# Optimization experiments

Hardware: AMD Instinct MI355X
Metric: run time of the kernel (lower is better)

Reference implementation:

```python
import jax, jax.numpy as jnp
import numpy as np

H = 16  # num_heads

def setup_inputs() -> dict:
    key = jax.random.key(0)
    k1, k2, k3 = jax.random.split(key, 3)
    D = 1024
    x = jax.random.normal(k1, (4, 2048, D), dtype=jnp.float32)
    W_qkv = jax.random.normal(k2, (D, 3 * D), dtype=jnp.float32) * (1.0 / np.sqrt(D))
    b_qkv = jnp.zeros((3 * D,), dtype=jnp.float32)
    W_out = jax.random.normal(k3, (D, D), dtype=jnp.float32) * (1.0 / np.sqrt(D))
    b_out = jnp.zeros((D,), dtype=jnp.float32)
    return {"x": x, "W_qkv": W_qkv, "b_qkv": b_qkv, "W_out": W_out, "b_out": b_out}

def reference(x, W_qkv, b_qkv, W_out, b_out):
    B, S, D = x.shape
    hd = D // H  # head_dim
    qkv = x @ W_qkv + b_qkv  # [B,S,3D]
    q, k, v = jnp.split(qkv, 3, axis=-1)
    # [B,S,D] -> [B,H,S,hd]
    q = q.reshape(B, S, H, hd).transpose(0, 2, 1, 3)
    k = k.reshape(B, S, H, hd).transpose(0, 2, 1, 3)
    v = v.reshape(B, S, H, hd).transpose(0, 2, 1, 3)
    scores = jnp.einsum('bhqd,bhkd->bhqk', q, k) / jnp.sqrt(jnp.float32(hd))
    weights = jax.nn.softmax(scores, axis=-1)  # dropout p=0.0 (eval)
    out = jnp.einsum('bhqk,bhkd->bhqd', weights, v)
    out = out.transpose(0, 2, 1, 3).reshape(B, S, D)
    return out @ W_out + b_out
```

## Files before the change

### kernel.cpp

```cpp
#include <hip/hip_runtime.h>

typedef __bf16 bf16;
typedef __bf16 bf16x4 __attribute__((ext_vector_type(4)));
typedef __bf16 bf16x8 __attribute__((ext_vector_type(8)));
typedef short s16x4 __attribute__((ext_vector_type(4)));
typedef float f32x4 __attribute__((ext_vector_type(4)));

static constexpr int NB = 4;
static constexpr int NS = 2048;
static constexpr int ND = 1024;
static constexpr int NH = 16;
static constexpr int HD = 64;
static constexpr float QSCALE = 0.18033688011112042f;

#define GL16(g, l)                                                             \
    __builtin_amdgcn_global_load_lds(                                          \
        (const __attribute__((address_space(1))) void*)(g),                    \
        (__attribute__((address_space(3))) void*)(l), 16, 0, 0)

static __device__ __forceinline__ unsigned pk2(float a, float b) {
    union { __bf16 h[2]; unsigned u; } t;
    t.h[0] = (__bf16)a; t.h[1] = (__bf16)b;
    return t.u;
}

__global__ void k_conv(const float* __restrict__ in, bf16* __restrict__ out, int n) {
    int i = (blockIdx.x * blockDim.x + threadIdx.x) * 4;
    if (i < n) {
        float4 v = *reinterpret_cast<const float4*>(in + i);
        bf16* o = out + i;
        o[0] = (bf16)v.x; o[1] = (bf16)v.y; o[2] = (bf16)v.z; o[3] = (bf16)v.w;
    }
}

__global__ void k_transconv(const float* __restrict__ in, bf16* __restrict__ out,
                            int K, int N) {
    __shared__ float tile[64][33];
    int k0 = blockIdx.y * 64, n0 = blockIdx.x * 32;
    int tx = threadIdx.x, ty = threadIdx.y;
#pragma unroll
    for (int i = 0; i < 8; ++i)
        tile[ty + 8 * i][tx] = in[(long)(k0 + ty + 8 * i) * N + n0 + tx];
    __syncthreads();
    int t = ty * 32 + tx;
    int row = t >> 3;
    int col8 = (t & 7) * 8;
    bf16x8 v;
#pragma unroll
    for (int c = 0; c < 8; ++c) v[c] = (bf16)tile[col8 + c][row];
    *reinterpret_cast<bf16x8*>(&out[(long)(n0 + row) * K + k0 + col8]) = v;
}

__global__ __launch_bounds__(256, 2) void k_gemmQKV(
    const bf16* __restrict__ A, const bf16* __restrict__ Bt,
    const float* __restrict__ bias,
    bf16* __restrict__ Qb, bf16* __restrict__ Kb, bf16* __restrict__ Vt,
    int Kd)
{
    constexpr int BM = 128, BN = 128, BK = 64;
    __shared__ __align__(16) bf16 As[2][BM * BK];
    __shared__ __align__(16) bf16 Bs[2][BN * BK];

    const int t = threadIdx.x;
    const int wid = t >> 6, lane = t & 63;
    const int wm = wid >> 1, wn = wid & 1;
    const int m0 = blockIdx.y * BM, n0 = blockIdx.x * BN;
    const int lrow = lane & 15, lhi = lane >> 4;

    const int srow0 = wid * 32 + (lane >> 3);
    const int scol = ((lane & 7) ^ (lane >> 3)) * 8;
    const bf16* ag = A + (long)(m0 + srow0) * Kd + scol;
    const bf16* bg = Bt + (long)(n0 + srow0) * Kd + scol;

    auto STAGE = [&](int buf_, int k0_) {
#pragma unroll
        for (int c = 0; c < 4; ++c) {
            GL16(ag + (long)(c * 8) * Kd + k0_, &As[buf_][(wid * 32 + c * 8) * BK]);
            GL16(bg + (long)(c * 8) * Kd + k0_, &Bs[buf_][(wid * 32 + c * 8) * BK]);
        }
    };

    f32x4 acc[4][4] = {};
    const int nt = Kd >> 6;
    const int swzr = (lrow & 7) << 4;
    int co[2];
#pragma unroll
    for (int kk = 0; kk < 2; ++kk)
        co[kk] = ((kk * 64 + lhi * 16) ^ swzr) >> 1;

    STAGE(0, 0);
    int cur = 0;
    for (int tix = 0; tix < nt; ++tix) {
        if (tix + 1 < nt) {
            STAGE(cur ^ 1, (tix + 1) * BK);
            asm volatile("s_waitcnt vmcnt(8)" ::: "memory");
        } else {
            asm volatile("s_waitcnt vmcnt(0)" ::: "memory");
        }
        __builtin_amdgcn_s_barrier();
        __builtin_amdgcn_sched_barrier(0);

        bf16x8 af[2][4], bfr[2][4];
#pragma unroll
        for (int kk = 0; kk < 2; ++kk)
#pragma unroll
            for (int i = 0; i < 4; ++i) {
                af[kk][i]  = *reinterpret_cast<const bf16x8*>(
                    &As[cur][(wm * 64 + i * 16 + lrow) * BK + co[kk]]);
                bfr[kk][i] = *reinterpret_cast<const bf16x8*>(
                    &Bs[cur][(wn * 64 + i * 16 + lrow) * BK + co[kk]]);
            }
        __builtin_amdgcn_s_setprio(1);
#pragma unroll
        for (int kk = 0; kk < 2; ++kk)
#pragma unroll
            for (int i = 0; i < 4; ++i)
#pragma unroll
                for (int j = 0; j < 4; ++j)
                    acc[i][j] = __builtin_amdgcn_mfma_f32_16x16x32_bf16(
                        bfr[kk][j], af[kk][i], acc[i][j], 0, 0, 0);
        __builtin_amdgcn_s_setprio(0);
        __builtin_amdgcn_s_barrier();
        cur ^= 1;
    }

    const int colbase = n0 + wn * 64;
    const int which = colbase >> 10;
    const bool isQ = (which == 0);

    bf16* eb = (bf16*)As + wid * 4096;
#pragma unroll
    for (int j = 0; j < 4; ++j) {
        f32x4 bv = *reinterpret_cast<const f32x4*>(&bias[colbase + j * 16 + 4 * lhi]);
#pragma unroll
        for (int i = 0; i < 4; ++i) {
            int srt = i * 16 + lrow;
            bf16x4 pk;
#pragma unroll
            for (int r = 0; r < 4; ++r) {
                float v = acc[i][j][r] + bv[r];
                pk[r] = (bf16)(isQ ? v * QSCALE : v);
            }
            *reinterpret_cast<bf16x4*>(
                reinterpret_cast<char*>(eb) + srt * 128 +
                (((j * 16 + 4 * lhi) * 2) ^ ((srt & 7) << 4))) = pk;
        }
    }
    const int h = (colbase & 1023) >> 6;
    const int mrow = m0 + wm * 64;
    const int bb = mrow >> 11, s0 = mrow & 2047;
    const long bh = (long)bb * NH + h;

    if (which < 2) {
        bf16* Ob = isQ ? Qb : Kb;
#pragma unroll
        for (int it = 0; it < 8; ++it) {
            int rt = it * 8 + (lane >> 3);
            bf16x8 v = *reinterpret_cast<const bf16x8*>(
                reinterpret_cast<char*>(eb) + rt * 128 +
                (((lane & 7) * 16) ^ ((rt & 7) << 4)));
            int s = s0 + rt;
            *reinterpret_cast<bf16x8*>(&Ob[(bh * NS + s) * HD + (lane & 7) * 8]) = v;
        }
    } else {
        const int p = (lane & 7) >> 2;
        const int l4 = (lane & 3) * 4;
        const int pos0 = (lane & 7) * 8;
#pragma unroll
        for (int it = 0; it < 8; ++it) {
            int dt = it * 8 + (lane >> 3);
            bf16x8 v;
#pragma unroll
            for (int j = 0; j < 8; ++j) {
                int k = 32 * p + 16 * (j >> 2) + l4 + (j & 3);
                v[j] = *reinterpret_cast<const bf16*>(
                    reinterpret_cast<char*>(eb) + k * 128 +
                    ((dt * 2) ^ ((k & 7) << 4)));
            }
            *reinterpret_cast<bf16x8*>(&Vt[(bh * HD + dt) * NS + s0 + pos0]) = v;
        }
    }
}

__global__ __launch_bounds__(256, 2) void k_gemmO(
    const bf16* __restrict__ A, const bf16* __restrict__ Bt,
    const float* __restrict__ bias, float* __restrict__ O, int Kd)
{
    constexpr int BM = 128, BN = 128, BK = 64;
    __shared__ __align__(16) bf16 As[2][BM * BK];
    __shared__ __align__(16) bf16 Bs[2][BN * BK];

    const int t = threadIdx.x;
    const int wid = t >> 6, lane = t & 63;
    const int wm = wid >> 1, wn = wid & 1;
    const int m0 = blockIdx.y * BM, n0 = blockIdx.x * BN;
    const int lrow = lane & 15, lhi = lane >> 4;

    const int srow0 = wid * 32 + (lane >> 3);
    const int scol = ((lane & 7) ^ (lane >> 3)) * 8;
    const bf16* ag = A + (long)(m0 + srow0) * Kd + scol;
    const bf16* bg = Bt + (long)(n0 + srow0) * Kd + scol;

    auto STAGE = [&](int buf_, int k0_) {
#pragma unroll
        for (int c = 0; c < 4; ++c) {
            GL16(ag + (long)(c * 8) * Kd + k0_, &As[buf_][(wid * 32 + c * 8) * BK]);
            GL16(bg + (long)(c * 8) * Kd + k0_, &Bs[buf_][(wid * 32 + c * 8) * BK]);
        }
    };

    f32x4 acc[4][4] = {};
    const int nt = Kd >> 6;
    const int swzr = (lrow & 7) << 4;
    int co[2];
#pragma unroll
    for (int kk = 0; kk < 2; ++kk)
        co[kk] = ((kk * 64 + lhi * 16) ^ swzr) >> 1;

    STAGE(0, 0);
    int cur = 0;
    for (int tix = 0; tix < nt; ++tix) {
        if (tix + 1 < nt) {
            STAGE(cur ^ 1, (tix + 1) * BK);
            asm volatile("s_waitcnt vmcnt(8)" ::: "memory");
        } else {
            asm volatile("s_waitcnt vmcnt(0)" ::: "memory");
        }
        __builtin_amdgcn_s_barrier();
        __builtin_amdgcn_sched_barrier(0);

        bf16x8 af[2][4], bfr[2][4];
#pragma unroll
        for (int kk = 0; kk < 2; ++kk)
#pragma unroll
            for (int i = 0; i < 4; ++i) {
                af[kk][i]  = *reinterpret_cast<const bf16x8*>(
                    &As[cur][(wm * 64 + i * 16 + lrow) * BK + co[kk]]);
                bfr[kk][i] = *reinterpret_cast<const bf16x8*>(
                    &Bs[cur][(wn * 64 + i * 16 + lrow) * BK + co[kk]]);
            }
        __builtin_amdgcn_s_setprio(1);
#pragma unroll
        for (int kk = 0; kk < 2; ++kk)
#pragma unroll
            for (int i = 0; i < 4; ++i)
#pragma unroll
                for (int j = 0; j < 4; ++j)
                    acc[i][j] = __builtin_amdgcn_mfma_f32_16x16x32_bf16(
                        bfr[kk][j], af[kk][i], acc[i][j], 0, 0, 0);
        __builtin_amdgcn_s_setprio(0);
        __builtin_amdgcn_s_barrier();
        cur ^= 1;
    }

    const int colbase = n0 + wn * 64;
    float* ef = (float*)As + wid * 2048;
#pragma unroll
    for (int half = 0; half < 2; ++half) {
#pragma unroll
        for (int i2 = 0; i2 < 2; ++i2) {
            int i = half * 2 + i2;
            int srt = i2 * 16 + lrow;
#pragma unroll
            for (int j = 0; j < 4; ++j) {
                f32x4 bv = *reinterpret_cast<const f32x4*>(
                    &bias[colbase + j * 16 + 4 * lhi]);
                f32x4 v = acc[i][j] + bv;
                *reinterpret_cast<f32x4*>(
                    reinterpret_cast<char*>(ef) + srt * 256 +
                    (((j * 16 + 4 * lhi) * 4) ^ ((srt & 7) << 4))) = v;
            }
        }
#pragma unroll
        for (int it = 0; it < 8; ++it) {
            int rt = it * 4 + (lane >> 4);
            f32x4 v = *reinterpret_cast<const f32x4*>(
                reinterpret_cast<char*>(ef) + rt * 256 +
                (((lane & 15) * 16) ^ ((rt & 7) << 4)));
            int row = m0 + wm * 64 + half * 32 + rt;
            *reinterpret_cast<f32x4*>(
                &O[(long)row * 1024 + colbase + (lane & 15) * 4]) = v;
        }
        asm volatile("" ::: "memory");
    }
}

__global__ __launch_bounds__(512, 4) void k_attn(
    const bf16* __restrict__ Qb, const bf16* __restrict__ Kb,
    const bf16* __restrict__ Vt, bf16* __restrict__ Ao)
{
    constexpr int KB = 64;
    constexpr int NT = NS / KB;
    __shared__ __align__(16) bf16 Ks[2][KB * HD];
    __shared__ __align__(16) bf16 Vs[2][HD * KB];

    const int t = threadIdx.x;
    const int wid = t >> 6, lane = t & 63;
    const int lrow = lane & 15, lhi = lane >> 4;

    const int flat = blockIdx.y * gridDim.x + blockIdx.x;
    const int n = (flat & 7) * 64 + (flat >> 3);
    const int bh = n >> 3;
    const int qw = (n & 7) * 256 + wid * 32;

    const bf16* Qg = Qb + ((long)bh * NS + qw) * HD;
    const bf16* Kg = Kb + (long)bh * NS * HD;
    const bf16* Vg = Vt + (long)bh * HD * NS;

    bf16x8 qf[2][2];
#pragma unroll
    for (int qfr = 0; qfr < 2; ++qfr)
#pragma unroll
        for (int c = 0; c < 2; ++c)
            qf[qfr][c] = *reinterpret_cast<const bf16x8*>(
                Qg + (long)(qfr * 16 + lrow) * HD + c * 32 + lhi * 8);

    f32x4 of[2][4] = {};
    float lsum[2] = {0.f, 0.f};

    const int gsr = lane >> 3;
    const int gsc = ((lane & 7) ^ gsr) * 8;
    const int rb = wid * 8;
    auto STAGE = [&](int buf, int kb) {
        GL16(Kg + (long)(kb + rb + gsr) * HD + gsc, &Ks[buf][rb * 64]);
        GL16(Vg + (long)(rb + gsr) * NS + kb + gsc, &Vs[buf][rb * 64]);
    };

    const int rsw = (lrow & 7) << 4;

    auto COMPUTE = [&](int b_) {
        f32x4 st[2][4] = {};
        __builtin_amdgcn_s_setprio(1);
#pragma unroll
        for (int j = 0; j < 4; ++j)
#pragma unroll
            for (int c = 0; c < 2; ++c) {
                bf16x8 kf = *reinterpret_cast<const bf16x8*>(
                    &Ks[b_][(j * 16 + lrow) * 64 + (((c * 64 + lhi * 16) ^ rsw) >> 1)]);
#pragma unroll
                for (int qfr = 0; qfr < 2; ++qfr)
                    st[qfr][j] = __builtin_amdgcn_mfma_f32_16x16x32_bf16(
                        kf, qf[qfr][c], st[qfr][j], 0, 0, 0);
            }
        __builtin_amdgcn_s_setprio(0);

        union { unsigned u[2]; s16x4 s; } pj[2][4];
#pragma unroll
        for (int qfr = 0; qfr < 2; ++qfr)
#pragma unroll
            for (int j = 0; j < 4; ++j) {
                float e0 = __builtin_amdgcn_exp2f(st[qfr][j][0]);
                float e1 = __builtin_amdgcn_exp2f(st[qfr][j][1]);
                float e2 = __builtin_amdgcn_exp2f(st[qfr][j][2]);
                float e3 = __builtin_amdgcn_exp2f(st[qfr][j][3]);
                lsum[qfr] += (e0 + e1) + (e2 + e3);
                pj[qfr][j].u[0] = pk2(e0, e1);
                pj[qfr][j].u[1] = pk2(e2, e3);
            }

        __builtin_amdgcn_s_setprio(1);
#pragma unroll
        for (int p = 0; p < 2; ++p)
#pragma unroll
            for (int f = 0; f < 4; ++f) {
                union { bf16x8 v; s16x4 h[2]; } vf;
                vf.v = *reinterpret_cast<const bf16x8*>(
                    &Vs[b_][(f * 16 + lrow) * 64 +
                            (((p * 64 + lhi * 16) ^ rsw) >> 1)]);
#pragma unroll
                for (int qfr = 0; qfr < 2; ++qfr) {
                    of[qfr][f] = __builtin_amdgcn_mfma_f32_16x16x16bf16_1k(
                        vf.h[0], pj[qfr][2 * p].s, of[qfr][f], 0, 0, 0);
                    of[qfr][f] = __builtin_amdgcn_mfma_f32_16x16x16bf16_1k(
                        vf.h[1], pj[qfr][2 * p + 1].s, of[qfr][f], 0, 0, 0);
                }
            }
        __builtin_amdgcn_s_setprio(0);
    };

    STAGE(0, 0);
    int cur = 0;
    for (int it = 0; it < NT; ++it) {
        if (it + 1 < NT) {
            STAGE(cur ^ 1, (it + 1) * KB);
            asm volatile("s_waitcnt vmcnt(2)" ::: "memory");
        } else {
            asm volatile("s_waitcnt vmcnt(0)" ::: "memory");
        }
        __builtin_amdgcn_s_barrier();
        __builtin_amdgcn_sched_barrier(0);
        COMPUTE(cur);
        __builtin_amdgcn_s_barrier();
        cur ^= 1;
    }

#pragma unroll
    for (int qfr = 0; qfr < 2; ++qfr) {
        lsum[qfr] += __shfl_xor(lsum[qfr], 16);
        lsum[qfr] += __shfl_xor(lsum[qfr], 32);
    }

    bf16* eb = (wid < 4) ? ((bf16*)Ks + wid * 2048) : ((bf16*)Vs + (wid - 4) * 2048);
#pragma unroll
    for (int qfr = 0; qfr < 2; ++qfr) {
        float inv = 1.0f / lsum[qfr];
        int srt = qfr * 16 + lrow;
#pragma unroll
        for (int f = 0; f < 4; ++f) {
            bf16x4 pk;
#pragma unroll
            for (int r = 0; r < 4; ++r) pk[r] = (bf16)(of[qfr][f][r] * inv);
            *reinterpret_cast<bf16x4*>(
                reinterpret_cast<char*>(eb) + srt * 128 +
                (((f * 16 + 4 * lhi) * 2) ^ ((srt & 7) << 4))) = pk;
        }
    }
    const int bb = bh >> 4, h = bh & 15;
#pragma unroll
    for (int it = 0; it < 4; ++it) {
        int rt = it * 8 + (lane >> 3);
        bf16x8 v = *reinterpret_cast<const bf16x8*>(
            reinterpret_cast<char*>(eb) + rt * 128 +
            (((lane & 7) * 16) ^ ((rt & 7) << 4)));
        int s = qw + rt;
        *reinterpret_cast<bf16x8*>(
            &Ao[((long)bb * NS + s) * ND + h * HD + (lane & 7) * 8]) = v;
    }
}

extern "C" void kernel_launch(void* const* d_in, const int* in_sizes, int n_in,
                              void* d_out, int out_size, void* d_ws, size_t ws_size,
                              hipStream_t stream) {
    const float* x    = (const float*)d_in[0];
    const float* Wqkv = (const float*)d_in[1];
    const float* bqkv = (const float*)d_in[2];
    const float* Wout = (const float*)d_in[3];
    const float* bout = (const float*)d_in[4];
    float* out = (float*)d_out;

    char* ws = (char*)d_ws;
    bf16* Xb  = (bf16*)(ws);
    bf16* Wqt = (bf16*)(ws + 16777216);
    bf16* Wot = (bf16*)(ws + 23068672);
    bf16* Qb  = (bf16*)(ws + 25165824);
    bf16* Kb  = (bf16*)(ws + 41943040);
    bf16* Vt  = (bf16*)(ws + 58720256);
    bf16* Ab  = (bf16*)(ws + 75497472);

    k_conv<<<dim3(8192), dim3(256), 0, stream>>>(x, Xb, NB * NS * ND);
    k_transconv<<<dim3(96, 16), dim3(32, 8), 0, stream>>>(Wqkv, Wqt, ND, 3 * ND);
    k_transconv<<<dim3(32, 16), dim3(32, 8), 0, stream>>>(Wout, Wot, ND, ND);

    k_gemmQKV<<<dim3(24, 64), dim3(256), 0, stream>>>(
        Xb, Wqt, bqkv, Qb, Kb, Vt, ND);

    k_attn<<<dim3(8, 64), dim3(512), 0, stream>>>(Qb, Kb, Vt, Ab);

    k_gemmO<<<dim3(8, 64), dim3(256), 0, stream>>>(
        Ab, Wot, bout, out, ND);
}
```

Measured before the change: 191.2 us.

## Switch attention kernel to 32x32x16 MFMA with permlane32 P-fragment swap

After: 192.5 us. About the same (+0.7%).

```diff
diff --git a/kernel.cpp b/kernel.cpp
--- a/kernel.cpp
+++ b/kernel.cpp
@@ -3,8 +3,9 @@
 typedef __bf16 bf16;
 typedef __bf16 bf16x4 __attribute__((ext_vector_type(4)));
 typedef __bf16 bf16x8 __attribute__((ext_vector_type(8)));
-typedef short s16x4 __attribute__((ext_vector_type(4)));
 typedef float f32x4 __attribute__((ext_vector_type(4)));
+typedef float f32x16 __attribute__((ext_vector_type(16)));
+typedef unsigned u32x2 __attribute__((ext_vector_type(2)));
 
 static constexpr int NB = 4;
 static constexpr int NS = 2048;
@@ -163,8 +164,6 @@
             *reinterpret_cast<bf16x8*>(&Ob[(bh * NS + s) * HD + (lane & 7) * 8]) = v;
         }
     } else {
-        const int p = (lane & 7) >> 2;
-        const int l4 = (lane & 3) * 4;
         const int pos0 = (lane & 7) * 8;
 #pragma unroll
         for (int it = 0; it < 8; ++it) {
@@ -172,10 +171,10 @@
             bf16x8 v;
 #pragma unroll
             for (int j = 0; j < 8; ++j) {
-                int k = 32 * p + 16 * (j >> 2) + l4 + (j & 3);
+                int s = pos0 + j;
                 v[j] = *reinterpret_cast<const bf16*>(
-                    reinterpret_cast<char*>(eb) + k * 128 +
-                    ((dt * 2) ^ ((k & 7) << 4)));
+                    reinterpret_cast<char*>(eb) + s * 128 +
+                    ((dt * 2) ^ ((s & 7) << 4)));
             }
             *reinterpret_cast<bf16x8*>(&Vt[(bh * HD + dt) * NS + s0 + pos0]) = v;
         }
@@ -296,7 +295,7 @@
 
     const int t = threadIdx.x;
     const int wid = t >> 6, lane = t & 63;
-    const int lrow = lane & 15, lhi = lane >> 4;
+    const int l31 = lane & 31, lh = lane >> 5;
 
     const int flat = blockIdx.y * gridDim.x + blockIdx.x;
     const int n = (flat & 7) * 64 + (flat >> 3);
@@ -307,16 +306,14 @@
     const bf16* Kg = Kb + (long)bh * NS * HD;
     const bf16* Vg = Vt + (long)bh * HD * NS;
 
-    bf16x8 qf[2][2];
-#pragma unroll
-    for (int qfr = 0; qfr < 2; ++qfr)
-#pragma unroll
-        for (int c = 0; c < 2; ++c)
-            qf[qfr][c] = *reinterpret_cast<const bf16x8*>(
-                Qg + (long)(qfr * 16 + lrow) * HD + c * 32 + lhi * 8);
-
-    f32x4 of[2][4] = {};
-    float lsum[2] = {0.f, 0.f};
+    bf16x8 qf[4];
+#pragma unroll
+    for (int kc = 0; kc < 4; ++kc)
+        qf[kc] = *reinterpret_cast<const bf16x8*>(
+            Qg + (long)l31 * HD + kc * 16 + 8 * lh);
+
+    f32x16 of0 = {}, of1 = {};
+    float lsum = 0.f;
 
     const int gsr = lane >> 3;
     const int gsc = ((lane & 7) ^ gsr) * 8;
@@ -326,55 +323,60 @@
         GL16(Vg + (long)(rb + gsr) * NS + kb + gsc, &Vs[buf][rb * 64]);
     };
 
-    const int rsw = (lrow & 7) << 4;
-
     auto COMPUTE = [&](int b_) {
-        f32x4 st[2][4] = {};
+        f32x16 st0 = {}, st1 = {};
         __builtin_amdgcn_s_setprio(1);
 #pragma unroll
-        for (int j = 0; j < 4; ++j)
-#pragma unroll
-            for (int c = 0; c < 2; ++c) {
-                bf16x8 kf = *reinterpret_cast<const bf16x8*>(
-                    &Ks[b_][(j * 16 + lrow) * 64 + (((c * 64 + lhi * 16) ^ rsw) >> 1)]);
-#pragma unroll
-                for (int qfr = 0; qfr < 2; ++qfr)
-                    st[qfr][j] = __builtin_amdgcn_mfma_f32_16x16x32_bf16(
-                        kf, qf[qfr][c], st[qfr][j], 0, 0, 0);
-            }
+        for (int kc = 0; kc < 4; ++kc) {
+            const int cb = (kc * 32 + 16 * lh);
+            const int r0 = l31, r1 = 32 + l31;
+            bf16x8 k0 = *reinterpret_cast<const bf16x8*>(
+                &Ks[b_][r0 * 64 + ((cb ^ ((r0 & 7) << 4)) >> 1)]);
+            bf16x8 k1 = *reinterpret_cast<const bf16x8*>(
+                &Ks[b_][r1 * 64 + ((cb ^ ((r1 & 7) << 4)) >> 1)]);
+            st0 = __builtin_amdgcn_mfma_f32_32x32x16_bf16(k0, qf[kc], st0, 0, 0, 0);
+            st1 = __builtin_amdgcn_mfma_f32_32x32x16_bf16(k1, qf[kc], st1, 0, 0, 0);
+        }
         __builtin_amdgcn_s_setprio(0);
 
-        union { unsigned u[2]; s16x4 s; } pj[2][4];
-#pragma unroll
-        for (int qfr = 0; qfr < 2; ++qfr)
-#pragma unroll
-            for (int j = 0; j < 4; ++j) {
-                float e0 = __builtin_amdgcn_exp2f(st[qfr][j][0]);
-                float e1 = __builtin_amdgcn_exp2f(st[qfr][j][1]);
-                float e2 = __builtin_amdgcn_exp2f(st[qfr][j][2]);
-                float e3 = __builtin_amdgcn_exp2f(st[qfr][j][3]);
-                lsum[qfr] += (e0 + e1) + (e2 + e3);
-                pj[qfr][j].u[0] = pk2(e0, e1);
-                pj[qfr][j].u[1] = pk2(e2, e3);
-            }
+        unsigned u0[4][2], u1[4][2];
+#pragma unroll
+        for (int g = 0; g < 4; ++g) {
+            float a0 = __builtin_amdgcn_exp2f(st0[4 * g]);
+            float a1 = __builtin_amdgcn_exp2f(st0[4 * g + 1]);
+            float a2 = __builtin_amdgcn_exp2f(st0[4 * g + 2]);
+            float a3 = __builtin_amdgcn_exp2f(st0[4 * g + 3]);
+            lsum += (a0 + a1) + (a2 + a3);
+            u0[g][0] = pk2(a0, a1); u0[g][1] = pk2(a2, a3);
+            float b0 = __builtin_amdgcn_exp2f(st1[4 * g]);
+            float b1 = __builtin_amdgcn_exp2f(st1[4 * g + 1]);
+            float b2 = __builtin_amdgcn_exp2f(st1[4 * g + 2]);
+            float b3 = __builtin_amdgcn_exp2f(st1[4 * g + 3]);
+            lsum += (b0 + b1) + (b2 + b3);
+            u1[g][0] = pk2(b0, b1); u1[g][1] = pk2(b2, b3);
+        }
 
         __builtin_amdgcn_s_setprio(1);
 #pragma unroll
-        for (int p = 0; p < 2; ++p)
-#pragma unroll
-            for (int f = 0; f < 4; ++f) {
-                union { bf16x8 v; s16x4 h[2]; } vf;
-                vf.v = *reinterpret_cast<const bf16x8*>(
-                    &Vs[b_][(f * 16 + lrow) * 64 +
-                            (((p * 64 + lhi * 16) ^ rsw) >> 1)]);
-#pragma unroll
-                for (int qfr = 0; qfr < 2; ++qfr) {
-                    of[qfr][f] = __builtin_amdgcn_mfma_f32_16x16x16bf16_1k(
-                        vf.h[0], pj[qfr][2 * p].s, of[qfr][f], 0, 0, 0);
-                    of[qfr][f] = __builtin_amdgcn_mfma_f32_16x16x16bf16_1k(
-                        vf.h[1], pj[qfr][2 * p + 1].s, of[qfr][f], 0, 0, 0);
-                }
-            }
+        for (int kc = 0; kc < 4; ++kc) {
+            const unsigned (*uu)[2] = (kc < 2) ? u0 : u1;
+            const int gl = 2 * (kc & 1), gh = gl + 1;
+            u32x2 sA = __builtin_amdgcn_permlane32_swap(uu[gl][0], uu[gh][0], false, false);
+            u32x2 sB = __builtin_amdgcn_permlane32_swap(uu[gl][1], uu[gh][1], false, false);
+            union { unsigned u[4]; bf16x8 v; } pf;
+            pf.u[0] = sA[0]; pf.u[1] = sB[0]; pf.u[2] = sA[1]; pf.u[3] = sB[1];
+            const int cb = kc * 32 + 16 * lh;
+#pragma unroll
+            for (int dt = 0; dt < 2; ++dt) {
+                const int row = dt * 32 + l31;
+                bf16x8 vf = *reinterpret_cast<const bf16x8*>(
+                    &Vs[b_][row * 64 + ((cb ^ ((row & 7) << 4)) >> 1)]);
+                if (dt == 0)
+                    of0 = __builtin_amdgcn_mfma_f32_32x32x16_bf16(vf, pf.v, of0, 0, 0, 0);
+                else
+                    of1 = __builtin_amdgcn_mfma_f32_32x32x16_bf16(vf, pf.v, of1, 0, 0, 0);
+            }
+        }
         __builtin_amdgcn_s_setprio(0);
     };
 
@@ -394,27 +396,26 @@
         cur ^= 1;
     }
 
-#pragma unroll
-    for (int qfr = 0; qfr < 2; ++qfr) {
-        lsum[qfr] += __shfl_xor(lsum[qfr], 16);
-        lsum[qfr] += __shfl_xor(lsum[qfr], 32);
-    }
+    lsum += __shfl_xor(lsum, 32);
+    const float inv = 1.0f / lsum;
 
     bf16* eb = (wid < 4) ? ((bf16*)Ks + wid * 2048) : ((bf16*)Vs + (wid - 4) * 2048);
-#pragma unroll
-    for (int qfr = 0; qfr < 2; ++qfr) {
-        float inv = 1.0f / lsum[qfr];
-        int srt = qfr * 16 + lrow;
-#pragma unroll
-        for (int f = 0; f < 4; ++f) {
+    const int qrow = l31;
+#pragma unroll
+    for (int dt = 0; dt < 2; ++dt)
+#pragma unroll
+        for (int g = 0; g < 4; ++g) {
             bf16x4 pk;
 #pragma unroll
-            for (int r = 0; r < 4; ++r) pk[r] = (bf16)(of[qfr][f][r] * inv);
+            for (int r = 0; r < 4; ++r) {
+                float v = (dt == 0) ? of0[4 * g + r] : of1[4 * g + r];
+                pk[r] = (bf16)(v * inv);
+            }
+            int d = dt * 32 + 8 * g + 4 * lh;
             *reinterpret_cast<bf16x4*>(
-                reinterpret_cast<char*>(eb) + srt * 128 +
-                (((f * 16 + 4 * lhi) * 2) ^ ((srt & 7) << 4))) = pk;
-        }
-    }
+                reinterpret_cast<char*>(eb) + qrow * 128 +
+                ((d * 2) ^ ((qrow & 7) << 4))) = pk;
+        }
     const int bb = bh >> 4, h = bh & 15;
 #pragma unroll
     for (int it = 0; it < 4; ++it) {
```
